# Performance work log

Hardware: AMD Instinct MI355X
Metric: run time of the kernel (lower is better)

## Reference

```python
import jax, jax.numpy as jnp
import numpy as np

DIMS = (2000, 500, 400)
H, DK, DV = 8, 32, 32
DM = H * DV  # 256
NUM_CLASS = 5
BS = 16384
TEMP = DK ** 0.5
LN_EPS = 1e-6


def setup_inputs() -> dict:
    key = jax.random.key(0)
    ks = jax.random.split(key, 32)
    inp = {"input_data": jax.random.normal(ks[0], (BS, sum(DIMS)), dtype=jnp.float32)}
    i = 1
    for name, odim in (("q", H * DK), ("k", H * DK), ("v", H * DV)):
        for m, d in enumerate(DIMS):
            inp[f"w{name}{m}"] = jax.random.normal(ks[i], (d, odim), dtype=jnp.float32) * (1.0 / np.sqrt(d)); i += 1
            inp[f"b{name}{m}"] = jnp.zeros((odim,), dtype=jnp.float32)
    inp["fc_w"] = jax.random.normal(ks[i], (DM, DM), dtype=jnp.float32) * (1.0 / np.sqrt(DM)); i += 1
    inp["fc_b"] = jnp.zeros((DM,), dtype=jnp.float32)
    inp["ln_g"] = jnp.ones((DM,), dtype=jnp.float32)
    inp["ln_b"] = jnp.zeros((DM,), dtype=jnp.float32)
    inp["out_w"] = jax.random.normal(ks[i], (len(DIMS) * DM, NUM_CLASS), dtype=jnp.float32) * (1.0 / np.sqrt(len(DIMS) * DM)); i += 1
    inp["out_b"] = jnp.zeros((NUM_CLASS,), dtype=jnp.float32)
    return inp


def _forward(input_data, wq, bq, wk, bk, wv, bv, fc_w, fc_b, ln_g, ln_b, out_w, out_b):
    bs = input_data.shape[0]
    M = len(DIMS)
    offs = np.concatenate([[0], np.cumsum(DIMS)])
    xs = [input_data[:, offs[m]:offs[m + 1]] for m in range(M)]
    # per-modality projections -> [bs, M, H*D]
    q = jnp.stack([xs[m] @ wq[m] + bq[m] for m in range(M)], axis=1)
    k = jnp.stack([xs[m] @ wk[m] + bk[m] for m in range(M)], axis=1)
    v = jnp.stack([xs[m] @ wv[m] + bv[m] for m in range(M)], axis=1)
    # [bs, H, M, D]
    qh = q.reshape(bs, M, H, DK).transpose(0, 2, 1, 3)
    kh = k.reshape(bs, M, H, DK).transpose(0, 2, 1, 3)
    vh = v.reshape(bs, M, H, DV).transpose(0, 2, 1, 3)
    attn = jnp.einsum("bhmd,bhnd->bhmn", qh / TEMP, kh)
    attn = attn / jnp.abs(attn.min())  # global-min scaling as in source
    attn = attn / jnp.maximum(jnp.sum(jnp.abs(attn), axis=-1, keepdims=True), 1e-12)  # L1 normalize
    attn = jax.nn.softmax(attn, axis=-1)
    o = jnp.einsum("bhmn,bhnd->bhmd", attn, vh)
    o = o.transpose(0, 2, 1, 3).reshape(bs, M, DM)
    residual = v  # [bs, M, DM]
    o = o @ fc_w + fc_b
    x = o + residual
    mu = x.mean(axis=-1, keepdims=True)
    var = ((x - mu) ** 2).mean(axis=-1, keepdims=True)
    x = (x - mu) / jnp.sqrt(var + LN_EPS) * ln_g + ln_b
    return x.reshape(bs, -1) @ out_w + out_b


def reference(input_data, wq0, bq0, wq1, bq1, wq2, bq2, wk0, bk0, wk1, bk1, wk2, bk2,
              wv0, bv0, wv1, bv1, wv2, bv2, fc_w, fc_b, ln_g, ln_b, out_w, out_b):
    return _forward(input_data, (wq0, wq1, wq2), (bq0, bq1, bq2), (wk0, wk1, wk2), (bk0, bk1, bk2),
                    (wv0, wv1, wv2), (bv0, bv1, bv2), fc_w, fc_b, ln_g, ln_b, out_w, out_b)
```

## Files before the change

kernel.cpp:

```cpp
#include <hip/hip_runtime.h>
#include <hip/hip_bf16.h>

#define BATCH 16384
#define HEADS 8
#define DDK 32
#define NQKV 768
#define NCLASS 5
#define LN_EPS 1e-6f

#define BM 128
#define BN 128
#define BKK 32

typedef _Float16 f16x8 __attribute__((ext_vector_type(8)));
typedef float f32x4 __attribute__((ext_vector_type(4)));

__device__ __forceinline__ void gl16(const void* g, void* l) {
    __builtin_amdgcn_global_load_lds(
        (const __attribute__((address_space(1))) unsigned int*)g,
        (__attribute__((address_space(3))) unsigned int*)l, 16, 0, 0);
}

__global__ __launch_bounds__(256) void convert_x_all(const float* __restrict__ X,
                                                     _Float16* __restrict__ A0,
                                                     _Float16* __restrict__ A1,
                                                     _Float16* __restrict__ A2,
                                                     int r0, int nrows) {
    const int total = nrows * 384;
    for (int i = blockIdx.x * blockDim.x + threadIdx.x; i < total;
         i += gridDim.x * blockDim.x) {
        const int rl = i / 384;
        const int slot = i - rl * 384;
        int k8, Kdim, xoff, lo_off;
        _Float16* dst;
        if (slot < 256) {
            k8 = slot << 3; Kdim = 2000; xoff = 0; lo_off = 2048;
            dst = A0 + (size_t)rl * 4096 + k8;
        } else if (slot < 320) {
            k8 = (slot - 256) << 3; Kdim = 500; xoff = 2000; lo_off = 512;
            dst = A1 + (size_t)rl * 1024 + k8;
        } else {
            k8 = (slot - 320) << 3; Kdim = 400; xoff = 2500; lo_off = 512;
            dst = A2 + (size_t)rl * 1024 + k8;
        }
        const float* src = X + (size_t)(r0 + rl) * 2900 + xoff + k8;
        float xv[8];
        if (k8 + 8 <= Kdim) {
            float4 v0 = *reinterpret_cast<const float4*>(src);
            float4 v1 = *reinterpret_cast<const float4*>(src + 4);
            xv[0] = v0.x; xv[1] = v0.y; xv[2] = v0.z; xv[3] = v0.w;
            xv[4] = v1.x; xv[5] = v1.y; xv[6] = v1.z; xv[7] = v1.w;
        } else {
#pragma unroll
            for (int j = 0; j < 8; ++j) xv[j] = (k8 + j < Kdim) ? src[j] : 0.f;
        }
        union { _Float16 h[8]; uint4 v; } hi, lo;
#pragma unroll
        for (int j = 0; j < 8; ++j) {
            hi.h[j] = (_Float16)xv[j];
            lo.h[j] = (_Float16)(xv[j] - (float)hi.h[j]);
        }
        *reinterpret_cast<uint4*>(dst) = hi.v;
        *reinterpret_cast<uint4*>(dst + lo_off) = lo.v;
    }
}

struct WArgs {
    const float* w[3][3];
    const float* b[3][3];
    const float* fcw;
    _Float16* Bt;
    float* biasx;
    _Float16* fcWh;
};

__global__ __launch_bounds__(256) void convert_w_all(WArgs a) {
    const int y = blockIdx.y;
    const int gid = blockIdx.x * 256 + threadIdx.x;
    if (y < 3) {
        const int m = y;
        const int Kdim = (m == 0) ? 2000 : (m == 1 ? 500 : 400);
        const int Kpad = (m == 0) ? 2048 : 512;
        if (gid < NQKV) {
            const int p = gid >> 8, c = gid & 255;
            a.biasx[m * NQKV + gid] = a.b[p][m][c];
        }
        _Float16* dst0 = a.Bt;
        if (m >= 1) dst0 += (size_t)NQKV * 4096;
        if (m == 2) dst0 += (size_t)NQKV * 1024;
        const int ld = 2 * Kpad;
        const int k8n = Kpad >> 3;
        const int total = NQKV * k8n;
        for (int i = gid; i < total; i += gridDim.x * 256) {
            const int kb = i / NQKV;
            const int n = i - kb * NQKV;
            const int k8 = kb << 3;
            const int p = n >> 8, c = n & 255;
            const float* wsrc = a.w[p][m];
            union { _Float16 h[8]; uint4 v; } hi;
#pragma unroll
            for (int j = 0; j < 8; ++j) {
                float x = (k8 + j < Kdim) ? wsrc[(size_t)(k8 + j) * 256 + c] : 0.f;
                hi.h[j] = (_Float16)x;
            }
            *reinterpret_cast<uint4*>(dst0 + (size_t)n * ld + k8) = hi.v;
            *reinterpret_cast<uint4*>(dst0 + (size_t)n * ld + Kpad + k8) = hi.v;
        }
    } else {
        for (int i = gid; i < 256 * 32; i += gridDim.x * 256) {
            const int n = i & 255;
            const int k8 = (i >> 8) << 3;
            union { _Float16 h[8]; uint4 v; } hi;
#pragma unroll
            for (int j = 0; j < 8; ++j)
                hi.h[j] = (_Float16)a.fcw[(size_t)(k8 + j) * 256 + n];
            *reinterpret_cast<uint4*>(a.fcWh + (size_t)n * 256 + k8) = hi.v;
        }
    }
}

struct GemmArgs {
    const _Float16* A[3];
    const _Float16* B[3];
    int keff[3];
};

__global__ __launch_bounds__(256) void qkv_mfma_all(
    GemmArgs ga, const float* __restrict__ biasx,
    float* __restrict__ Qo, float* __restrict__ Ko, float* __restrict__ Vo,
    int r0) {
    const int z = blockIdx.z;
    const _Float16* __restrict__ A = ga.A[z];
    const _Float16* __restrict__ Bt = ga.B[z];
    const int ld = ga.keff[z];
    const int nk = ld >> 5;
    const float* __restrict__ bias = biasx + z * NQKV;

    const int row0l = blockIdx.x * BM;
    const int nb = blockIdx.y * BN;
    const int tid = threadIdx.x;
    const int lane = tid & 63;
    const int w = tid >> 6;
    const int wr = w >> 1, wc = w & 1;

    __shared__ alignas(16) _Float16 As[BM * BKK];
    __shared__ alignas(16) _Float16 Bs[BN * BKK];

    f32x4 acc[4][4];
#pragma unroll
    for (int i = 0; i < 4; ++i)
#pragma unroll
        for (int j = 0; j < 4; ++j) acc[i][j] = (f32x4){0.f, 0.f, 0.f, 0.f};

    const int rs = lane >> 2;
    const int kk = (lane & 3) * 8;
    const size_t gA0 = (size_t)(row0l + w * 16 + rs) * ld + kk;
    const size_t gA1 = gA0 + (size_t)64 * ld;
    const size_t gB0 = (size_t)(nb + w * 16 + rs) * ld + kk;
    const size_t gB1 = gB0 + (size_t)64 * ld;
    _Float16* lA0 = &As[(w * 16) * BKK];
    _Float16* lA1 = &As[(64 + w * 16) * BKK];
    _Float16* lB0 = &Bs[(w * 16) * BKK];
    _Float16* lB1 = &Bs[(64 + w * 16) * BKK];

    const int fr = lane & 15;
    const int fk = (lane >> 4) * 8;
    const int aoff0 = (wr * 64 + fr) * BKK + fk;
    const int boff0 = (wc * 64 + fr) * BKK + fk;

#pragma unroll 1
    for (int kt = 0; kt < nk; ++kt) {
        const int k0 = kt * BKK;
        __syncthreads();
        gl16(A + gA0 + k0, lA0);
        gl16(A + gA1 + k0, lA1);
        gl16(Bt + gB0 + k0, lB0);
        gl16(Bt + gB1 + k0, lB1);
        __syncthreads();

        f16x8 a[4], b[4];
#pragma unroll
        for (int mi = 0; mi < 4; ++mi)
            a[mi] = *reinterpret_cast<const f16x8*>(&As[aoff0 + mi * 16 * BKK]);
#pragma unroll
        for (int ni = 0; ni < 4; ++ni)
            b[ni] = *reinterpret_cast<const f16x8*>(&Bs[boff0 + ni * 16 * BKK]);
#pragma unroll
        for (int mi = 0; mi < 4; ++mi)
#pragma unroll
            for (int ni = 0; ni < 4; ++ni)
                acc[mi][ni] = __builtin_amdgcn_mfma_f32_16x16x32_f16(
                    a[mi], b[ni], acc[mi][ni], 0, 0, 0);
    }

#pragma unroll
    for (int ni = 0; ni < 4; ++ni) {
        const int gc = nb + wc * 64 + ni * 16 + fr;
        const int proj = gc >> 8;
        const int col = gc & 255;
        const float bv = bias[gc];
        float* outp = (proj == 0 ? Qo : proj == 1 ? Ko : Vo);
#pragma unroll
        for (int mi = 0; mi < 4; ++mi) {
            const int gr = r0 + row0l + wr * 64 + mi * 16 + (lane >> 4) * 4;
            float* p = outp + (size_t)gr * NQKV + z * 256 + col;
#pragma unroll
            for (int j = 0; j < 4; ++j)
                p[(size_t)j * NQKV] = acc[mi][ni][j] + bv;
        }
    }
}

__global__ __launch_bounds__(256) void attn_kernel(const float* __restrict__ Q,
                                                   const float* __restrict__ K,
                                                   const float* __restrict__ V,
                                                   _Float16* __restrict__ Of) {
    const int s = blockIdx.x;
    const int t = threadIdx.x;
    __shared__ float qs[NQKV], ks[NQKV], vs[NQKV];
    __shared__ float att[HEADS][3][3];

    const size_t base = (size_t)s * NQKV;
    for (int i = t; i < NQKV; i += 256) {
        qs[i] = Q[base + i];
        ks[i] = K[base + i];
        vs[i] = V[base + i];
    }
    __syncthreads();

    if (t < 72) {
        const int h = t / 9, ij = t % 9, i = ij / 3, j = ij % 3;
        const float* qp = &qs[i * 256 + h * 32];
        const float* kp = &ks[j * 256 + h * 32];
        float sc = 0.f;
#pragma unroll
        for (int d = 0; d < DDK; ++d) sc = fmaf(qp[d], kp[d], sc);
        att[h][i][j] = sc;
    }
    __syncthreads();
    if (t < 24) {
        const int h = t / 3, i = t % 3;
        float s0 = att[h][i][0], s1 = att[h][i][1], s2 = att[h][i][2];
        float r = fabsf(s0) + fabsf(s1) + fabsf(s2);
        r = fmaxf(r, 1e-12f);
        float p0 = s0 / r, p1 = s1 / r, p2 = s2 / r;
        float mx = fmaxf(p0, fmaxf(p1, p2));
        float e0 = expf(p0 - mx), e1 = expf(p1 - mx), e2 = expf(p2 - mx);
        float inv = 1.f / (e0 + e1 + e2);
        att[h][i][0] = e0 * inv;
        att[h][i][1] = e1 * inv;
        att[h][i][2] = e2 * inv;
    }
    __syncthreads();

    const int c = t;
    const int h = c >> 5;
#pragma unroll
    for (int m = 0; m < 3; ++m) {
        float o = att[h][m][0] * vs[c] + att[h][m][1] * vs[256 + c] + att[h][m][2] * vs[512 + c];
        const size_t ob = ((size_t)s * 3 + m) * 512 + c;
        _Float16 oh = (_Float16)o;
        Of[ob] = oh;
        Of[ob + 256] = (_Float16)(o - (float)oh);
    }
}

__global__ __launch_bounds__(256) void fc_mfma(const _Float16* __restrict__ O,
                                               const _Float16* __restrict__ Wh,
                                               const float* __restrict__ fcb,
                                               const float* __restrict__ resid,
                                               float* __restrict__ X) {
    const int row0 = blockIdx.x * BM;
    const int nb = blockIdx.y * BN;
    const int tid = threadIdx.x;
    const int lane = tid & 63;
    const int w = tid >> 6;
    const int wr = w >> 1, wc = w & 1;

    __shared__ alignas(16) _Float16 AsH[BM * BKK];
    __shared__ alignas(16) _Float16 AsL[BM * BKK];
    __shared__ alignas(16) _Float16 BsH[BN * BKK];

    f32x4 acc[4][4];
#pragma unroll
    for (int i = 0; i < 4; ++i)
#pragma unroll
        for (int j = 0; j < 4; ++j) acc[i][j] = (f32x4){0.f, 0.f, 0.f, 0.f};

    const int rs = lane >> 2;
    const int kk = (lane & 3) * 8;
    const size_t gA0 = (size_t)(row0 + w * 16 + rs) * 512 + kk;
    const size_t gA1 = (size_t)(row0 + (w + 4) * 16 + rs) * 512 + kk;
    const size_t gB0 = (size_t)(nb + w * 16 + rs) * 256 + kk;
    const size_t gB1 = (size_t)(nb + (w + 4) * 16 + rs) * 256 + kk;
    _Float16* lAH0 = &AsH[w * 512];
    _Float16* lAH1 = &AsH[(w + 4) * 512];
    _Float16* lAL0 = &AsL[w * 512];
    _Float16* lAL1 = &AsL[(w + 4) * 512];
    _Float16* lBH0 = &BsH[w * 512];
    _Float16* lBH1 = &BsH[(w + 4) * 512];

    const int fr = lane & 15;
    const int fk = (lane >> 4) * 8;
    const int aoff0 = (wr * 64 + fr) * BKK + fk;
    const int boff0 = (wc * 64 + fr) * BKK + fk;

#pragma unroll 1
    for (int kt = 0; kt < 8; ++kt) {
        const int k0 = kt * BKK;
        __syncthreads();
        gl16(O + gA0 + k0, lAH0);
        gl16(O + gA1 + k0, lAH1);
        gl16(O + 256 + gA0 + k0, lAL0);
        gl16(O + 256 + gA1 + k0, lAL1);
        gl16(Wh + gB0 + k0, lBH0);
        gl16(Wh + gB1 + k0, lBH1);
        __syncthreads();

        f16x8 ah[4], bh[4];
#pragma unroll
        for (int mi = 0; mi < 4; ++mi)
            ah[mi] = *reinterpret_cast<const f16x8*>(&AsH[aoff0 + mi * 16 * BKK]);
#pragma unroll
        for (int ni = 0; ni < 4; ++ni)
            bh[ni] = *reinterpret_cast<const f16x8*>(&BsH[boff0 + ni * 16 * BKK]);
#pragma unroll
        for (int mi = 0; mi < 4; ++mi)
#pragma unroll
            for (int ni = 0; ni < 4; ++ni)
                acc[mi][ni] = __builtin_amdgcn_mfma_f32_16x16x32_f16(
                    ah[mi], bh[ni], acc[mi][ni], 0, 0, 0);
        {
            f16x8 al[4];
#pragma unroll
            for (int mi = 0; mi < 4; ++mi)
                al[mi] = *reinterpret_cast<const f16x8*>(&AsL[aoff0 + mi * 16 * BKK]);
#pragma unroll
            for (int mi = 0; mi < 4; ++mi)
#pragma unroll
                for (int ni = 0; ni < 4; ++ni)
                    acc[mi][ni] = __builtin_amdgcn_mfma_f32_16x16x32_f16(
                        al[mi], bh[ni], acc[mi][ni], 0, 0, 0);
        }
    }

#pragma unroll
    for (int ni = 0; ni < 4; ++ni) {
        const int gc = nb + wc * 64 + ni * 16 + fr;
        const float bv = fcb[gc];
#pragma unroll
        for (int mi = 0; mi < 4; ++mi) {
            const int gr = row0 + wr * 64 + mi * 16 + (lane >> 4) * 4;
#pragma unroll
            for (int j = 0; j < 4; ++j) {
                const size_t off = (size_t)(gr + j) * 256 + gc;
                X[off] = acc[mi][ni][j] + bv + resid[off];
            }
        }
    }
}

__global__ __launch_bounds__(256) void ln_out_kernel(const float* __restrict__ X,
                                                     const float* __restrict__ g,
                                                     const float* __restrict__ bb,
                                                     const float* __restrict__ ow,
                                                     const float* __restrict__ ob,
                                                     float* __restrict__ out) {
    const int s = blockIdx.x;
    const int t = threadIdx.x;
    const int lane = t & 63, wv = t >> 6;
    __shared__ float xr[NQKV];
    __shared__ float red1[4], red2[4];
    __shared__ float cpart[4][NCLASS];

    const size_t base = (size_t)s * NQKV;
    const float gg = g[t];
    const float bbv = bb[t];

    for (int m = 0; m < 3; ++m) {
        float v = X[base + m * 256 + t];
        float s1 = v, s2 = v * v;
#pragma unroll
        for (int off = 32; off > 0; off >>= 1) {
            s1 += __shfl_down(s1, off);
            s2 += __shfl_down(s2, off);
        }
        if (lane == 0) { red1[wv] = s1; red2[wv] = s2; }
        __syncthreads();
        const float tot = red1[0] + red1[1] + red1[2] + red1[3];
        const float tot2 = red2[0] + red2[1] + red2[2] + red2[3];
        const float mu = tot * (1.f / 256.f);
        const float var = tot2 * (1.f / 256.f) - mu * mu;
        const float inv = 1.0f / sqrtf(var + LN_EPS);
        xr[m * 256 + t] = (v - mu) * inv * gg + bbv;
        __syncthreads();
    }

    float p[NCLASS] = {0.f, 0.f, 0.f, 0.f, 0.f};
    for (int i = t; i < NQKV; i += 256) {
        const float xv = xr[i];
#pragma unroll
        for (int c = 0; c < NCLASS; ++c) p[c] = fmaf(xv, ow[i * NCLASS + c], p[c]);
    }
#pragma unroll
    for (int c = 0; c < NCLASS; ++c) {
        float pv = p[c];
#pragma unroll
        for (int off = 32; off > 0; off >>= 1) pv += __shfl_down(pv, off);
        if (lane == 0) cpart[wv][c] = pv;
    }
    __syncthreads();
    if (t < NCLASS)
        out[(size_t)s * NCLASS + t] =
            cpart[0][t] + cpart[1][t] + cpart[2][t] + cpart[3][t] + ob[t];
}

extern "C" void kernel_launch(void* const* d_in, const int* in_sizes, int n_in,
                              void* d_out, int out_size, void* d_ws, size_t ws_size,
                              hipStream_t stream) {
    const float* x = (const float*)d_in[0];
    WArgs wa;
    int idx = 1;
    for (int p = 0; p < 3; ++p)
        for (int m = 0; m < 3; ++m) {
            wa.w[p][m] = (const float*)d_in[idx++];
            wa.b[p][m] = (const float*)d_in[idx++];
        }
    const float* fc_w = (const float*)d_in[19];
    const float* fc_b = (const float*)d_in[20];
    const float* ln_g = (const float*)d_in[21];
    const float* ln_b = (const float*)d_in[22];
    const float* out_w = (const float*)d_in[23];
    const float* out_b = (const float*)d_in[24];

    float* ws = (float*)d_ws;
    const size_t SZ = (size_t)BATCH * NQKV;
    float* Q = ws;
    float* Kb = ws + SZ;
    float* Vb = ws + 2 * SZ;
    float* biasx = ws + 3 * SZ;
    _Float16* Bt = (_Float16*)(biasx + 3 * NQKV);
    _Float16* fcWh = Bt + (size_t)NQKV * 6144;
    _Float16* pool = fcWh + 256 * 256;

    wa.fcw = fc_w; wa.Bt = Bt; wa.biasx = biasx; wa.fcWh = fcWh;

    const size_t fixed_bytes = (size_t)((char*)pool - (char*)d_ws);
    const size_t avail = (ws_size > fixed_bytes) ? ws_size - fixed_bytes : 0;
    size_t rc = (avail / 12288) & ~(size_t)127;
    if (rc < 128) rc = 128;
    if (rc > BATCH) rc = BATCH;
    const int rows_chunk = (int)rc;

    float* X = Q;
    _Float16* Of = pool;

    convert_w_all<<<dim3(768, 4), 256, 0, stream>>>(wa);

    GemmArgs ga;
    ga.keff[0] = 4096; ga.keff[1] = 1024; ga.keff[2] = 1024;
    ga.B[0] = Bt;
    ga.B[1] = Bt + (size_t)NQKV * 4096;
    ga.B[2] = Bt + (size_t)NQKV * 5120;

    _Float16* A0 = pool;
    _Float16* A1 = A0 + (size_t)rows_chunk * 4096;
    _Float16* A2 = A1 + (size_t)rows_chunk * 1024;
    ga.A[0] = A0; ga.A[1] = A1; ga.A[2] = A2;

    for (int r0 = 0; r0 < BATCH; r0 += rows_chunk) {
        const int nr = (BATCH - r0 < rows_chunk) ? (BATCH - r0) : rows_chunk;
        const int cgrid = (nr * 384 + 255) / 256;
        convert_x_all<<<(cgrid < 2048 ? cgrid : 2048), 256, 0, stream>>>(
            x, A0, A1, A2, r0, nr);
        dim3 g(nr / BM, NQKV / BN, 3);
        qkv_mfma_all<<<g, 256, 0, stream>>>(ga, biasx, Q, Kb, Vb, r0);
    }

    attn_kernel<<<BATCH, 256, 0, stream>>>(Q, Kb, Vb, Of);

    fc_mfma<<<dim3((BATCH * 3) / BM, 2), 256, 0, stream>>>(Of, fcWh, fc_b, Vb, X);

    ln_out_kernel<<<BATCH, 256, 0, stream>>>(X, ln_g, ln_b, out_w, out_b, (float*)d_out);
}
```

Baseline: 706.5 us.

## Fuse fp32-to-fp16 hi/lo input split into QKV MFMA GEMM with register prefetch

```diff
diff --git a/kernel.cpp b/kernel.cpp
--- a/kernel.cpp
+++ b/kernel.cpp
@@ -19,50 +19,6 @@
     __builtin_amdgcn_global_load_lds(
         (const __attribute__((address_space(1))) unsigned int*)g,
         (__attribute__((address_space(3))) unsigned int*)l, 16, 0, 0);
-}
-
-__global__ __launch_bounds__(256) void convert_x_all(const float* __restrict__ X,
-                                                     _Float16* __restrict__ A0,
-                                                     _Float16* __restrict__ A1,
-                                                     _Float16* __restrict__ A2,
-                                                     int r0, int nrows) {
-    const int total = nrows * 384;
-    for (int i = blockIdx.x * blockDim.x + threadIdx.x; i < total;
-         i += gridDim.x * blockDim.x) {
-        const int rl = i / 384;
-        const int slot = i - rl * 384;
-        int k8, Kdim, xoff, lo_off;
-        _Float16* dst;
-        if (slot < 256) {
-            k8 = slot << 3; Kdim = 2000; xoff = 0; lo_off = 2048;
-            dst = A0 + (size_t)rl * 4096 + k8;
-        } else if (slot < 320) {
-            k8 = (slot - 256) << 3; Kdim = 500; xoff = 2000; lo_off = 512;
-            dst = A1 + (size_t)rl * 1024 + k8;
-        } else {
-            k8 = (slot - 320) << 3; Kdim = 400; xoff = 2500; lo_off = 512;
-            dst = A2 + (size_t)rl * 1024 + k8;
-        }
-        const float* src = X + (size_t)(r0 + rl) * 2900 + xoff + k8;
-        float xv[8];
-        if (k8 + 8 <= Kdim) {
-            float4 v0 = *reinterpret_cast<const float4*>(src);
-            float4 v1 = *reinterpret_cast<const float4*>(src + 4);
-            xv[0] = v0.x; xv[1] = v0.y; xv[2] = v0.z; xv[3] = v0.w;
-            xv[4] = v1.x; xv[5] = v1.y; xv[6] = v1.z; xv[7] = v1.w;
-        } else {
-#pragma unroll
-            for (int j = 0; j < 8; ++j) xv[j] = (k8 + j < Kdim) ? src[j] : 0.f;
-        }
-        union { _Float16 h[8]; uint4 v; } hi, lo;
-#pragma unroll
-        for (int j = 0; j < 8; ++j) {
-            hi.h[j] = (_Float16)xv[j];
-            lo.h[j] = (_Float16)(xv[j] - (float)hi.h[j]);
-        }
-        *reinterpret_cast<uint4*>(dst) = hi.v;
-        *reinterpret_cast<uint4*>(dst + lo_off) = lo.v;
-    }
 }
 
 struct WArgs {
@@ -86,9 +42,8 @@
             a.biasx[m * NQKV + gid] = a.b[p][m][c];
         }
         _Float16* dst0 = a.Bt;
-        if (m >= 1) dst0 += (size_t)NQKV * 4096;
-        if (m == 2) dst0 += (size_t)NQKV * 1024;
-        const int ld = 2 * Kpad;
+        if (m >= 1) dst0 += (size_t)NQKV * 2048;
+        if (m == 2) dst0 += (size_t)NQKV * 512;
         const int k8n = Kpad >> 3;
         const int total = NQKV * k8n;
         for (int i = gid; i < total; i += gridDim.x * 256) {
@@ -103,8 +58,7 @@
                 float x = (k8 + j < Kdim) ? wsrc[(size_t)(k8 + j) * 256 + c] : 0.f;
                 hi.h[j] = (_Float16)x;
             }
-            *reinterpret_cast<uint4*>(dst0 + (size_t)n * ld + k8) = hi.v;
-            *reinterpret_cast<uint4*>(dst0 + (size_t)n * ld + Kpad + k8) = hi.v;
+            *reinterpret_cast<uint4*>(dst0 + (size_t)n * Kpad + k8) = hi.v;
         }
     } else {
         for (int i = gid; i < 256 * 32; i += gridDim.x * 256) {
@@ -120,20 +74,68 @@
 }
 
 struct GemmArgs {
-    const _Float16* A[3];
+    const float* X;
     const _Float16* B[3];
-    int keff[3];
+    int ldB[3];
+    int nk[3];
+    int Kd[3];
+    int xoff[3];
 };
+
+struct Aregs { float4 v[4]; };
+
+__device__ __forceinline__ void loadA(const float* xbase, int k0, int Kd, int kh,
+                                      Aregs& R) {
+    if (k0 + 32 <= Kd) {
+#pragma unroll
+        for (int j = 0; j < 4; ++j)
+            R.v[j] = *reinterpret_cast<const float4*>(xbase + k0 + j * 4);
+    } else {
+#pragma unroll
+        for (int j = 0; j < 4; ++j) {
+            float4 t = make_float4(0.f, 0.f, 0.f, 0.f);
+            const int kb = k0 + kh + j * 4;
+            if (kb + 0 < Kd) t.x = xbase[k0 + j * 4 + 0];
+            if (kb + 1 < Kd) t.y = xbase[k0 + j * 4 + 1];
+            if (kb + 2 < Kd) t.z = xbase[k0 + j * 4 + 2];
+            if (kb + 3 < Kd) t.w = xbase[k0 + j * 4 + 3];
+            R.v[j] = t;
+        }
+    }
+}
+
+__device__ __forceinline__ void cvtSplit(const Aregs& R, uint4& h0, uint4& h1,
+                                         uint4& l0, uint4& l1) {
+    union { _Float16 h[8]; uint4 v; } H0, H1, L0, L1;
+    float f[16];
+#pragma unroll
+    for (int j = 0; j < 4; ++j) {
+        f[j * 4 + 0] = R.v[j].x; f[j * 4 + 1] = R.v[j].y;
+        f[j * 4 + 2] = R.v[j].z; f[j * 4 + 3] = R.v[j].w;
+    }
+#pragma unroll
+    for (int e = 0; e < 8; ++e) {
+        _Float16 h = (_Float16)f[e];
+        H0.h[e] = h;
+        L0.h[e] = (_Float16)(f[e] - (float)h);
+    }
+#pragma unroll
+    for (int e = 0; e < 8; ++e) {
+        _Float16 h = (_Float16)f[8 + e];
+        H1.h[e] = h;
+        L1.h[e] = (_Float16)(f[8 + e] - (float)h);
+    }
+    h0 = H0.v; h1 = H1.v; l0 = L0.v; l1 = L1.v;
+}
 
 __global__ __launch_bounds__(256) void qkv_mfma_all(
     GemmArgs ga, const float* __restrict__ biasx,
-    float* __restrict__ Qo, float* __restrict__ Ko, float* __restrict__ Vo,
-    int r0) {
+    float* __restrict__ Qo, float* __restrict__ Ko, float* __restrict__ Vo) {
     const int z = blockIdx.z;
-    const _Float16* __restrict__ A = ga.A[z];
     const _Float16* __restrict__ Bt = ga.B[z];
-    const int ld = ga.keff[z];
-    const int nk = ld >> 5;
+    const int ldB = ga.ldB[z];
+    const int nkz = ga.nk[z];
+    const int Kd = ga.Kd[z];
     const float* __restrict__ bias = biasx + z * NQKV;
 
     const int row0l = blockIdx.x * BM;
@@ -143,7 +145,8 @@
     const int w = tid >> 6;
     const int wr = w >> 1, wc = w & 1;
 
-    __shared__ alignas(16) _Float16 As[BM * BKK];
+    __shared__ alignas(16) _Float16 AsH[BM * BKK];
+    __shared__ alignas(16) _Float16 AsL[BM * BKK];
     __shared__ alignas(16) _Float16 Bs[BN * BKK];
 
     f32x4 acc[4][4];
@@ -152,45 +155,101 @@
 #pragma unroll
         for (int j = 0; j < 4; ++j) acc[i][j] = (f32x4){0.f, 0.f, 0.f, 0.f};
 
+    const int ar = tid >> 1;
+    const int kh = (tid & 1) * 16;
+    const float* xbase = ga.X + (size_t)(row0l + ar) * 2900 + ga.xoff[z] + kh;
+    uint4* wrH = reinterpret_cast<uint4*>(&AsH[tid * 16]);
+    uint4* wrL = reinterpret_cast<uint4*>(&AsL[tid * 16]);
+
     const int rs = lane >> 2;
-    const int kk = (lane & 3) * 8;
-    const size_t gA0 = (size_t)(row0l + w * 16 + rs) * ld + kk;
-    const size_t gA1 = gA0 + (size_t)64 * ld;
-    const size_t gB0 = (size_t)(nb + w * 16 + rs) * ld + kk;
-    const size_t gB1 = gB0 + (size_t)64 * ld;
-    _Float16* lA0 = &As[(w * 16) * BKK];
-    _Float16* lA1 = &As[(64 + w * 16) * BKK];
+    const int kkv = (lane & 3) * 8;
+    const size_t gB0 = (size_t)(nb + w * 16 + rs) * ldB + kkv;
+    const size_t gB1 = (size_t)(nb + (w + 4) * 16 + rs) * ldB + kkv;
     _Float16* lB0 = &Bs[(w * 16) * BKK];
-    _Float16* lB1 = &Bs[(64 + w * 16) * BKK];
+    _Float16* lB1 = &Bs[((w + 4) * 16) * BKK];
 
     const int fr = lane & 15;
     const int fk = (lane >> 4) * 8;
     const int aoff0 = (wr * 64 + fr) * BKK + fk;
     const int boff0 = (wc * 64 + fr) * BKK + fk;
 
+    Aregs RA, RB;
+    uint4 pAh0, pAh1, pAl0, pAl1;
+    uint4 pBh0, pBh1, pBl0, pBl1;
+
+    loadA(xbase, 0, Kd, kh, RA);
+    cvtSplit(RA, pAh0, pAh1, pAl0, pAl1);
+
 #pragma unroll 1
-    for (int kt = 0; kt < nk; ++kt) {
-        const int k0 = kt * BKK;
-        __syncthreads();
-        gl16(A + gA0 + k0, lA0);
-        gl16(A + gA1 + k0, lA1);
-        gl16(Bt + gB0 + k0, lB0);
-        gl16(Bt + gB1 + k0, lB1);
-        __syncthreads();
-
-        f16x8 a[4], b[4];
-#pragma unroll
-        for (int mi = 0; mi < 4; ++mi)
-            a[mi] = *reinterpret_cast<const f16x8*>(&As[aoff0 + mi * 16 * BKK]);
-#pragma unroll
-        for (int ni = 0; ni < 4; ++ni)
-            b[ni] = *reinterpret_cast<const f16x8*>(&Bs[boff0 + ni * 16 * BKK]);
-#pragma unroll
-        for (int mi = 0; mi < 4; ++mi)
+    for (int kt = 0; kt < nkz; kt += 2) {
+        {
+            const int k0 = kt * BKK;
+            __syncthreads();
+            wrH[0] = pAh0; wrH[1] = pAh1;
+            wrL[0] = pAl0; wrL[1] = pAl1;
+            gl16(Bt + gB0 + k0, lB0);
+            gl16(Bt + gB1 + k0, lB1);
+            __syncthreads();
+            loadA(xbase, (kt + 1) * BKK, Kd, kh, RB);
+            f16x8 b[4];
 #pragma unroll
             for (int ni = 0; ni < 4; ++ni)
-                acc[mi][ni] = __builtin_amdgcn_mfma_f32_16x16x32_f16(
-                    a[mi], b[ni], acc[mi][ni], 0, 0, 0);
+                b[ni] = *reinterpret_cast<const f16x8*>(&Bs[boff0 + ni * 16 * BKK]);
+            f16x8 a[4];
+#pragma unroll
+            for (int mi = 0; mi < 4; ++mi)
+                a[mi] = *reinterpret_cast<const f16x8*>(&AsH[aoff0 + mi * 16 * BKK]);
+#pragma unroll
+            for (int mi = 0; mi < 4; ++mi)
+#pragma unroll
+                for (int ni = 0; ni < 4; ++ni)
+                    acc[mi][ni] = __builtin_amdgcn_mfma_f32_16x16x32_f16(
+                        a[mi], b[ni], acc[mi][ni], 0, 0, 0);
+#pragma unroll
+            for (int mi = 0; mi < 4; ++mi)
+                a[mi] = *reinterpret_cast<const f16x8*>(&AsL[aoff0 + mi * 16 * BKK]);
+#pragma unroll
+            for (int mi = 0; mi < 4; ++mi)
+#pragma unroll
+                for (int ni = 0; ni < 4; ++ni)
+                    acc[mi][ni] = __builtin_amdgcn_mfma_f32_16x16x32_f16(
+                        a[mi], b[ni], acc[mi][ni], 0, 0, 0);
+            cvtSplit(RB, pBh0, pBh1, pBl0, pBl1);
+        }
+        {
+            const int k0 = (kt + 1) * BKK;
+            __syncthreads();
+            wrH[0] = pBh0; wrH[1] = pBh1;
+            wrL[0] = pBl0; wrL[1] = pBl1;
+            gl16(Bt + gB0 + k0, lB0);
+            gl16(Bt + gB1 + k0, lB1);
+            __syncthreads();
+            if (kt + 2 < nkz) loadA(xbase, (kt + 2) * BKK, Kd, kh, RA);
+            f16x8 b[4];
+#pragma unroll
+            for (int ni = 0; ni < 4; ++ni)
+                b[ni] = *reinterpret_cast<const f16x8*>(&Bs[boff0 + ni * 16 * BKK]);
+            f16x8 a[4];
+#pragma unroll
+            for (int mi = 0; mi < 4; ++mi)
+                a[mi] = *reinterpret_cast<const f16x8*>(&AsH[aoff0 + mi * 16 * BKK]);
+#pragma unroll
+            for (int mi = 0; mi < 4; ++mi)
+#pragma unroll
+                for (int ni = 0; ni < 4; ++ni)
+                    acc[mi][ni] = __builtin_amdgcn_mfma_f32_16x16x32_f16(
+                        a[mi], b[ni], acc[mi][ni], 0, 0, 0);
+#pragma unroll
+            for (int mi = 0; mi < 4; ++mi)
+                a[mi] = *reinterpret_cast<const f16x8*>(&AsL[aoff0 + mi * 16 * BKK]);
+#pragma unroll
+            for (int mi = 0; mi < 4; ++mi)
+#pragma unroll
+                for (int ni = 0; ni < 4; ++ni)
+                    acc[mi][ni] = __builtin_amdgcn_mfma_f32_16x16x32_f16(
+                        a[mi], b[ni], acc[mi][ni], 0, 0, 0);
+            cvtSplit(RA, pAh0, pAh1, pAl0, pAl1);
+        }
     }
 
 #pragma unroll
@@ -202,7 +261,7 @@
         float* outp = (proj == 0 ? Qo : proj == 1 ? Ko : Vo);
 #pragma unroll
         for (int mi = 0; mi < 4; ++mi) {
-            const int gr = r0 + row0l + wr * 64 + mi * 16 + (lane >> 4) * 4;
+            const int gr = row0l + wr * 64 + mi * 16 + (lane >> 4) * 4;
             float* p = outp + (size_t)gr * NQKV + z * 256 + col;
 #pragma unroll
             for (int j = 0; j < 4; ++j)
@@ -440,42 +499,27 @@
     float* Vb = ws + 2 * SZ;
     float* biasx = ws + 3 * SZ;
     _Float16* Bt = (_Float16*)(biasx + 3 * NQKV);
-    _Float16* fcWh = Bt + (size_t)NQKV * 6144;
-    _Float16* pool = fcWh + 256 * 256;
+    _Float16* fcWh = Bt + (size_t)NQKV * 3072;
+    _Float16* Of = fcWh + 256 * 256;
 
     wa.fcw = fc_w; wa.Bt = Bt; wa.biasx = biasx; wa.fcWh = fcWh;
 
-    const size_t fixed_bytes = (size_t)((char*)pool - (char*)d_ws);
-    const size_t avail = (ws_size > fixed_bytes) ? ws_size - fixed_bytes : 0;
-    size_t rc = (avail / 12288) & ~(size_t)127;
-    if (rc < 128) rc = 128;
-    if (rc > BATCH) rc = BATCH;
-    const int rows_chunk = (int)rc;
-
     float* X = Q;
-    _Float16* Of = pool;
 
     convert_w_all<<<dim3(768, 4), 256, 0, stream>>>(wa);
 
     GemmArgs ga;
-    ga.keff[0] = 4096; ga.keff[1] = 1024; ga.keff[2] = 1024;
+    ga.X = x;
     ga.B[0] = Bt;
-    ga.B[1] = Bt + (size_t)NQKV * 4096;
-    ga.B[2] = Bt + (size_t)NQKV * 5120;
-
-    _Float16* A0 = pool;
-    _Float16* A1 = A0 + (size_t)rows_chunk * 4096;
-    _Float16* A2 = A1 + (size_t)rows_chunk * 1024;
-    ga.A[0] = A0; ga.A[1] = A1; ga.A[2] = A2;
-
-    for (int r0 = 0; r0 < BATCH; r0 += rows_chunk) {
-        const int nr = (BATCH - r0 < rows_chunk) ? (BATCH - r0) : rows_chunk;
-        const int cgrid = (nr * 384 + 255) / 256;
-        convert_x_all<<<(cgrid < 2048 ? cgrid : 2048), 256, 0, stream>>>(
-            x, A0, A1, A2, r0, nr);
-        dim3 g(nr / BM, NQKV / BN, 3);
-        qkv_mfma_all<<<g, 256, 0, stream>>>(ga, biasx, Q, Kb, Vb, r0);
-    }
+    ga.B[1] = Bt + (size_t)NQKV * 2048;
+    ga.B[2] = Bt + (size_t)NQKV * 2048 + (size_t)NQKV * 512;
+    ga.ldB[0] = 2048; ga.ldB[1] = 512; ga.ldB[2] = 512;
+    ga.nk[0] = 64; ga.nk[1] = 16; ga.nk[2] = 14;
+    ga.Kd[0] = 2000; ga.Kd[1] = 500; ga.Kd[2] = 400;
+    ga.xoff[0] = 0; ga.xoff[1] = 2000; ga.xoff[2] = 2500;
+
+    dim3 g(BATCH / BM, NQKV / BN, 3);
+    qkv_mfma_all<<<g, 256, 0, stream>>>(ga, biasx, Q, Kb, Vb);
 
     attn_kernel<<<BATCH, 256, 0, stream>>>(Q, Kb, Vb, Of);
 
```

Result: faster. 654.9 us (-7.3%).
